# Kernel tuning notes

Measured on AMD Instinct MI355X. Metric: run time of the kernel, lower is better.

The kernel has to match this reference:

```python
import jax, jax.numpy as jnp
import numpy as np

C = 8      # num_channels
H = 512    # dim_hidden
B, S = 32, 1024
EPS = 1e-5


def _layernorm(x, gamma, beta):
    mu = jnp.mean(x, axis=-1, keepdims=True)
    var = jnp.var(x, axis=-1, keepdims=True)
    return (x - mu) * jax.lax.rsqrt(var + EPS) * gamma + beta


def setup_inputs() -> dict:
    key = jax.random.key(0)
    ks = jax.random.split(key, 7)
    x = jax.random.normal(ks[0], (C, B, S, 1), dtype=jnp.float32)
    # per-channel Linear(1,H): torch weight [H,1] -> stacked as [C,H]
    enc_w = jax.random.normal(ks[1], (C, H), dtype=jnp.float32) / jnp.sqrt(1.0)
    enc_b = jax.random.normal(ks[2], (C, H), dtype=jnp.float32) * 0.02
    enc_gamma = jnp.ones((C, H), dtype=jnp.float32)
    enc_beta = jnp.zeros((C, H), dtype=jnp.float32)
    # modulator Linear(C*H -> H): torch weight [H, C*H]
    mod_w = jax.random.normal(ks[3], (H, C * H), dtype=jnp.float32) / jnp.sqrt(C * H)
    mod_b = jax.random.normal(ks[4], (H,), dtype=jnp.float32) * 0.02
    mod_gamma = jnp.ones((H,), dtype=jnp.float32)
    mod_beta = jnp.zeros((H,), dtype=jnp.float32)
    return {
        "x": x,
        "enc_w": enc_w, "enc_b": enc_b,
        "enc_gamma": enc_gamma, "enc_beta": enc_beta,
        "mod_w": mod_w, "mod_b": mod_b,
        "mod_gamma": mod_gamma, "mod_beta": mod_beta,
    }


def reference(x, enc_w, enc_b, enc_gamma, enc_beta, mod_w, mod_b, mod_gamma, mod_beta):
    # per-channel Linear(1,H): h[c,b,s,:] = x[c,b,s,0]*enc_w[c] + enc_b[c]
    h = x * enc_w[:, None, None, :] + enc_b[:, None, None, :]      # [C,B,S,H]
    h = _layernorm(h, enc_gamma[:, None, None, :], enc_beta[:, None, None, :])
    h = jax.nn.gelu(h, approximate=False)
    # concat along last dim in channel order -> [B,S,C*H]
    h = jnp.transpose(h, (1, 2, 0, 3)).reshape(B, S, C * H)
    # channel modulator: Linear + LayerNorm + GELU
    y = jnp.einsum("bsk,hk->bsh", h, mod_w) + mod_b                # [B,S,H]
    y = _layernorm(y, mod_gamma, mod_beta)
    return jax.nn.gelu(y, approximate=False)
```

## Files before the change

kernel.cpp:

```cpp
#include <hip/hip_runtime.h>
#include <hip/hip_bf16.h>
#include <math.h>

#define C_CH 8
#define H_DIM 512
#define BS 32768
#define K_DIM 4096
#define EPS 1e-5f

#define TM 64
#define TK 32
#define NKT (K_DIM / TK)

typedef __bf16 bf16x8 __attribute__((ext_vector_type(8)));
typedef float  floatx4 __attribute__((ext_vector_type(4)));

__device__ __forceinline__ float gelu_fast(float v) {
    float x = v * fmaf(v * v, 0.07135481627f, 1.595769122f);
    float e = __expf(-x);
    return v * __builtin_amdgcn_rcpf(1.0f + e);
}

__global__ __launch_bounds__(256) void conv_w_kernel(const float* __restrict__ w,
                                                     __bf16* __restrict__ o) {
    int gtid  = blockIdx.x * 256 + threadIdx.x;
    int lane  = gtid & 63;
    int chunk = gtid >> 6;
    int kt    = chunk >> 5;
    int ntile = chunk & 31;
    int col   = ntile * 16 + (lane & 15);
    int k     = kt * 32 + (lane >> 4) * 8;
    const float* src = w + (size_t)col * K_DIM + k;
    float4 a = *(const float4*)src;
    float4 b = *(const float4*)(src + 4);
    bf16x8 h;
    h[0] = (__bf16)a.x; h[1] = (__bf16)a.y; h[2] = (__bf16)a.z; h[3] = (__bf16)a.w;
    h[4] = (__bf16)b.x; h[5] = (__bf16)b.y; h[6] = (__bf16)b.z; h[7] = (__bf16)b.w;
    *(bf16x8*)(o + (size_t)gtid * 8) = h;
}

template <int USE_WS>
__global__ __launch_bounds__(256, 2) void fused_gemm_kernel(
    const float* __restrict__ x,
    const float* __restrict__ enc_w,
    const float* __restrict__ enc_b,
    const float* __restrict__ enc_gamma,
    const float* __restrict__ enc_beta,
    const float* __restrict__ mod_w,
    const __bf16* __restrict__ Wb,
    const float* __restrict__ mod_b,
    const float* __restrict__ mod_gamma,
    const float* __restrict__ mod_beta,
    float* __restrict__ out)
{
    __shared__ float stats[C_CH][5];
    __shared__ float pS[C_CH][TM];
    __shared__ float qS[C_CH][TM];
    __shared__ float rS[C_CH][TM];
    __shared__ __align__(16) __bf16 Als[2][TM * TK];
    __shared__ float redS[TM][4];
    __shared__ float redQ[TM][4];
    __shared__ float muS[TM];
    __shared__ float invS[TM];

    const int tid  = threadIdx.x;
    const int wave = tid >> 6;
    const int lane = tid & 63;

    for (int c = wave; c < C_CH; c += 4) {
        float sw = 0.f, sb = 0.f, sww = 0.f, sbb = 0.f, swb = 0.f;
        for (int j = lane; j < H_DIM; j += 64) {
            float w = enc_w[c * H_DIM + j];
            float b = enc_b[c * H_DIM + j];
            sw += w; sb += b;
            sww = fmaf(w, w, sww);
            sbb = fmaf(b, b, sbb);
            swb = fmaf(w, b, swb);
        }
        #pragma unroll
        for (int off = 32; off; off >>= 1) {
            sw  += __shfl_xor(sw,  off);
            sb  += __shfl_xor(sb,  off);
            sww += __shfl_xor(sww, off);
            sbb += __shfl_xor(sbb, off);
            swb += __shfl_xor(swb, off);
        }
        if (lane == 0) {
            const float inv = 1.0f / (float)H_DIM;
            float mw = sw * inv, mb = sb * inv;
            stats[c][0] = mw;
            stats[c][1] = mb;
            stats[c][2] = sww * inv - mw * mw;
            stats[c][3] = sbb * inv - mb * mb;
            stats[c][4] = swb * inv - mw * mb;
        }
    }
    __syncthreads();

    const int row0 = blockIdx.x * TM;
    for (int idx = tid; idx < C_CH * TM; idx += 256) {
        int c = idx >> 6;
        int m = idx & (TM - 1);
        float xv = x[c * BS + row0 + m];
        float mw = stats[c][0], mb = stats[c][1];
        float vw = stats[c][2], vb = stats[c][3], cwb = stats[c][4];
        float var = fmaf(xv, fmaf(xv, vw, 2.0f * cwb), vb);
        float q = rsqrtf(var + EPS);
        float p = xv * q;
        pS[c][m] = p;
        qS[c][m] = q;
        rS[c][m] = -fmaf(p, mw, q * mb);
    }
    __syncthreads();

    const int wn = wave;
    const int lr = lane & 15;
    const int lq = lane >> 4;

    const int arow = tid >> 2;
    const int aq   = tid & 3;
    const int wchunk = arow * 4 + (aq ^ ((arow >> 1) & 3));

    floatx4 acc[4][8];
    #pragma unroll
    for (int i = 0; i < 4; ++i)
        #pragma unroll
        for (int j = 0; j < 8; ++j)
            acc[i][j] = (floatx4){0.f, 0.f, 0.f, 0.f};

    auto stageA = [&](int ktn, __bf16* dst) {
        const int k0 = ktn * TK;
        const int c  = k0 >> 9;
        const int j0 = c * H_DIM + (k0 & (H_DIM - 1)) + aq * 8;
        float p = pS[c][arow], q = qS[c][arow], r = rS[c][arow];
        bf16x8 hv;
        #pragma unroll
        for (int h = 0; h < 2; ++h) {
            float4 w = *(const float4*)(enc_w + j0 + h * 4);
            float4 b = *(const float4*)(enc_b + j0 + h * 4);
            float4 g = *(const float4*)(enc_gamma + j0 + h * 4);
            float4 e = *(const float4*)(enc_beta + j0 + h * 4);
            float fw[4] = {w.x, w.y, w.z, w.w};
            float fb[4] = {b.x, b.y, b.z, b.w};
            float fg[4] = {g.x, g.y, g.z, g.w};
            float fe[4] = {e.x, e.y, e.z, e.w};
            #pragma unroll
            for (int i = 0; i < 4; ++i) {
                float t = fmaf(p, fw[i], fmaf(q, fb[i], r));
                float v = fmaf(t, fg[i], fe[i]);
                hv[h * 4 + i] = (__bf16)gelu_fast(v);
            }
        }
        *(bf16x8*)(dst + wchunk * 8) = hv;
    };

    auto loadB = [&](int ktn, int half, bf16x8* dst) {
        if (USE_WS) {
            const __bf16* base = Wb + ((size_t)(ktn * 32 + wn * 8 + half * 4) * 64 + lane) * 8;
            #pragma unroll
            for (int nt = 0; nt < 4; ++nt)
                dst[nt] = *(const bf16x8*)(base + (size_t)nt * 64 * 8);
        } else {
            const int kk = ktn * 32 + lq * 8;
            #pragma unroll
            for (int nt = 0; nt < 4; ++nt) {
                int col = wn * 128 + (half * 4 + nt) * 16 + lr;
                const float* src = mod_w + (size_t)col * K_DIM + kk;
                float4 a = *(const float4*)src;
                float4 b = *(const float4*)(src + 4);
                bf16x8 h;
                h[0] = (__bf16)a.x; h[1] = (__bf16)a.y; h[2] = (__bf16)a.z; h[3] = (__bf16)a.w;
                h[4] = (__bf16)b.x; h[5] = (__bf16)b.y; h[6] = (__bf16)b.z; h[7] = (__bf16)b.w;
                dst[nt] = h;
            }
        }
    };

    bf16x8 bfrP[4], bfrQ[4];
    loadB(0, 0, bfrP);
    stageA(0, Als[0]);
    __syncthreads();

    for (int kt = 0; kt < NKT; ++kt) {
        loadB(kt, 1, bfrQ);

        if (kt + 1 < NKT) stageA(kt + 1, Als[(kt + 1) & 1]);

        const __bf16* Acur = Als[kt & 1];
        bf16x8 af[4];
        #pragma unroll
        for (int mt = 0; mt < 4; ++mt) {
            int row = mt * 16 + lr;
            int chunk = row * 4 + (lq ^ ((row >> 1) & 3));
            af[mt] = *(const bf16x8*)(Acur + chunk * 8);
        }

        #pragma unroll
        for (int mt = 0; mt < 4; ++mt)
            #pragma unroll
            for (int nt = 0; nt < 4; ++nt)
                acc[mt][nt] = __builtin_amdgcn_mfma_f32_16x16x32_bf16(
                    af[mt], bfrP[nt], acc[mt][nt], 0, 0, 0);

        if (kt + 1 < NKT) loadB(kt + 1, 0, bfrP);

        #pragma unroll
        for (int mt = 0; mt < 4; ++mt)
            #pragma unroll
            for (int nt = 0; nt < 4; ++nt)
                acc[mt][nt + 4] = __builtin_amdgcn_mfma_f32_16x16x32_bf16(
                    af[mt], bfrQ[nt], acc[mt][nt + 4], 0, 0, 0);

        __syncthreads();
    }

    float mbv[8], gv[8], bev[8];
    #pragma unroll
    for (int nt = 0; nt < 8; ++nt) {
        int col = wn * 128 + nt * 16 + lr;
        mbv[nt] = mod_b[col];
        gv[nt]  = mod_gamma[col];
        bev[nt] = mod_beta[col];
    }
    #pragma unroll
    for (int mt = 0; mt < 4; ++mt)
        #pragma unroll
        for (int nt = 0; nt < 8; ++nt)
            #pragma unroll
            for (int r = 0; r < 4; ++r)
                acc[mt][nt][r] += mbv[nt];

    #pragma unroll
    for (int mt = 0; mt < 4; ++mt) {
        #pragma unroll
        for (int r = 0; r < 4; ++r) {
            float s = 0.f, ss = 0.f;
            #pragma unroll
            for (int nt = 0; nt < 8; ++nt) {
                float y = acc[mt][nt][r];
                s += y;
                ss = fmaf(y, y, ss);
            }
            #pragma unroll
            for (int off = 1; off < 16; off <<= 1) {
                s  += __shfl_xor(s,  off);
                ss += __shfl_xor(ss, off);
            }
            if (lr == 0) {
                int row = mt * 16 + lq * 4 + r;
                redS[row][wn] = s;
                redQ[row][wn] = ss;
            }
        }
    }
    __syncthreads();
    if (tid < TM) {
        float s  = redS[tid][0] + redS[tid][1] + redS[tid][2] + redS[tid][3];
        float ss = redQ[tid][0] + redQ[tid][1] + redQ[tid][2] + redQ[tid][3];
        const float inv_n = 1.0f / (float)H_DIM;
        float mu  = s * inv_n;
        float var = ss * inv_n - mu * mu;
        muS[tid]  = mu;
        invS[tid] = rsqrtf(var + EPS);
    }
    __syncthreads();

    #pragma unroll
    for (int mt = 0; mt < 4; ++mt) {
        #pragma unroll
        for (int r = 0; r < 4; ++r) {
            int row = mt * 16 + lq * 4 + r;
            float mu  = muS[row];
            float inv = invS[row];
            float* op = out + (size_t)(row0 + row) * H_DIM;
            #pragma unroll
            for (int nt = 0; nt < 8; ++nt) {
                int col = wn * 128 + nt * 16 + lr;
                float t = fmaf((acc[mt][nt][r] - mu) * inv, gv[nt], bev[nt]);
                op[col] = gelu_fast(t);
            }
        }
    }
}

extern "C" void kernel_launch(void* const* d_in, const int* in_sizes, int n_in,
                              void* d_out, int out_size, void* d_ws, size_t ws_size,
                              hipStream_t stream) {
    const float* x         = (const float*)d_in[0];
    const float* enc_w     = (const float*)d_in[1];
    const float* enc_b     = (const float*)d_in[2];
    const float* enc_gamma = (const float*)d_in[3];
    const float* enc_beta  = (const float*)d_in[4];
    const float* mod_w     = (const float*)d_in[5];
    const float* mod_b     = (const float*)d_in[6];
    const float* mod_gamma = (const float*)d_in[7];
    const float* mod_beta  = (const float*)d_in[8];
    float* out = (float*)d_out;

    const size_t wb_bytes = (size_t)H_DIM * K_DIM * sizeof(__bf16);
    int use_ws = (ws_size >= wb_bytes) ? 1 : 0;
    __bf16* Wb = (__bf16*)d_ws;

    if (use_ws) {
        conv_w_kernel<<<(H_DIM * K_DIM) / (256 * 8), 256, 0, stream>>>(mod_w, Wb);
        fused_gemm_kernel<1><<<BS / TM, 256, 0, stream>>>(
            x, enc_w, enc_b, enc_gamma, enc_beta, mod_w, Wb,
            mod_b, mod_gamma, mod_beta, out);
    } else {
        fused_gemm_kernel<0><<<BS / TM, 256, 0, stream>>>(
            x, enc_w, enc_b, enc_gamma, enc_beta, mod_w, Wb,
            mod_b, mod_gamma, mod_beta, out);
    }
}
```

Measured before the change: 278.0 us.

## Split GEMM block across eight waves, each owning 64 output columns

The block grows from 256 to 512 threads so each of eight waves computes a 64x64 slice of the output instead of four waves computing 64x128. The per-wave accumulator drops from 32 to 16 MFMA tiles. The A-staging, stats and LayerNorm reductions are remapped so each thread does half the work. The goal is fewer registers and more resident waves to hide latency, at the cost of more A-fragment LDS reads per output and more threads per barrier.

```diff
diff --git a/kernel.cpp b/kernel.cpp
--- a/kernel.cpp
+++ b/kernel.cpp
@@ -13,6 +13,7 @@
 #define NKT (K_DIM / TK)
 
 typedef __bf16 bf16x8 __attribute__((ext_vector_type(8)));
+typedef __bf16 bf16x4 __attribute__((ext_vector_type(4)));
 typedef float  floatx4 __attribute__((ext_vector_type(4)));
 
 __device__ __forceinline__ float gelu_fast(float v) {
@@ -40,7 +41,7 @@
 }
 
 template <int USE_WS>
-__global__ __launch_bounds__(256, 2) void fused_gemm_kernel(
+__global__ __launch_bounds__(512, 4) void fused_gemm_kernel(
     const float* __restrict__ x,
     const float* __restrict__ enc_w,
     const float* __restrict__ enc_b,
@@ -58,8 +59,8 @@
     __shared__ float qS[C_CH][TM];
     __shared__ float rS[C_CH][TM];
     __shared__ __align__(16) __bf16 Als[2][TM * TK];
-    __shared__ float redS[TM][4];
-    __shared__ float redQ[TM][4];
+    __shared__ float redS[TM][8];
+    __shared__ float redQ[TM][8];
     __shared__ float muS[TM];
     __shared__ float invS[TM];
 
@@ -67,7 +68,8 @@
     const int wave = tid >> 6;
     const int lane = tid & 63;
 
-    for (int c = wave; c < C_CH; c += 4) {
+    {
+        const int c = wave;
         float sw = 0.f, sb = 0.f, sww = 0.f, sbb = 0.f, swb = 0.f;
         for (int j = lane; j < H_DIM; j += 64) {
             float w = enc_w[c * H_DIM + j];
@@ -98,9 +100,9 @@
     __syncthreads();
 
     const int row0 = blockIdx.x * TM;
-    for (int idx = tid; idx < C_CH * TM; idx += 256) {
-        int c = idx >> 6;
-        int m = idx & (TM - 1);
+    {
+        int c = wave;
+        int m = lane;
         float xv = x[c * BS + row0 + m];
         float mw = stats[c][0], mb = stats[c][1];
         float vw = stats[c][2], vb = stats[c][3], cwb = stats[c][4];
@@ -117,54 +119,51 @@
     const int lr = lane & 15;
     const int lq = lane >> 4;
 
-    const int arow = tid >> 2;
-    const int aq   = tid & 3;
-    const int wchunk = arow * 4 + (aq ^ ((arow >> 1) & 3));
-
-    floatx4 acc[4][8];
+    const int arow  = tid >> 3;
+    const int akq   = (tid >> 1) & 3;
+    const int ahalf = tid & 1;
+    const int wchunk = arow * 4 + (akq ^ ((arow >> 1) & 3));
+
+    floatx4 acc[4][4];
     #pragma unroll
     for (int i = 0; i < 4; ++i)
         #pragma unroll
-        for (int j = 0; j < 8; ++j)
+        for (int j = 0; j < 4; ++j)
             acc[i][j] = (floatx4){0.f, 0.f, 0.f, 0.f};
 
     auto stageA = [&](int ktn, __bf16* dst) {
         const int k0 = ktn * TK;
         const int c  = k0 >> 9;
-        const int j0 = c * H_DIM + (k0 & (H_DIM - 1)) + aq * 8;
+        const int j0 = c * H_DIM + (k0 & (H_DIM - 1)) + akq * 8 + ahalf * 4;
         float p = pS[c][arow], q = qS[c][arow], r = rS[c][arow];
-        bf16x8 hv;
-        #pragma unroll
-        for (int h = 0; h < 2; ++h) {
-            float4 w = *(const float4*)(enc_w + j0 + h * 4);
-            float4 b = *(const float4*)(enc_b + j0 + h * 4);
-            float4 g = *(const float4*)(enc_gamma + j0 + h * 4);
-            float4 e = *(const float4*)(enc_beta + j0 + h * 4);
-            float fw[4] = {w.x, w.y, w.z, w.w};
-            float fb[4] = {b.x, b.y, b.z, b.w};
-            float fg[4] = {g.x, g.y, g.z, g.w};
-            float fe[4] = {e.x, e.y, e.z, e.w};
-            #pragma unroll
-            for (int i = 0; i < 4; ++i) {
-                float t = fmaf(p, fw[i], fmaf(q, fb[i], r));
-                float v = fmaf(t, fg[i], fe[i]);
-                hv[h * 4 + i] = (__bf16)gelu_fast(v);
-            }
-        }
-        *(bf16x8*)(dst + wchunk * 8) = hv;
+        float4 w = *(const float4*)(enc_w + j0);
+        float4 b = *(const float4*)(enc_b + j0);
+        float4 g = *(const float4*)(enc_gamma + j0);
+        float4 e = *(const float4*)(enc_beta + j0);
+        float fw[4] = {w.x, w.y, w.z, w.w};
+        float fb[4] = {b.x, b.y, b.z, b.w};
+        float fg[4] = {g.x, g.y, g.z, g.w};
+        float fe[4] = {e.x, e.y, e.z, e.w};
+        bf16x4 hv;
+        #pragma unroll
+        for (int i = 0; i < 4; ++i) {
+            float t = fmaf(p, fw[i], fmaf(q, fb[i], r));
+            float v = fmaf(t, fg[i], fe[i]);
+            hv[i] = (__bf16)gelu_fast(v);
+        }
+        *(bf16x4*)(dst + wchunk * 8 + ahalf * 4) = hv;
     };
 
     auto loadB = [&](int ktn, int half, bf16x8* dst) {
         if (USE_WS) {
-            const __bf16* base = Wb + ((size_t)(ktn * 32 + wn * 8 + half * 4) * 64 + lane) * 8;
-            #pragma unroll
-            for (int nt = 0; nt < 4; ++nt)
-                dst[nt] = *(const bf16x8*)(base + (size_t)nt * 64 * 8);
+            const __bf16* base = Wb + ((size_t)(ktn * 32 + wn * 4 + half * 2) * 64 + lane) * 8;
+            dst[0] = *(const bf16x8*)(base);
+            dst[1] = *(const bf16x8*)(base + 512);
         } else {
             const int kk = ktn * 32 + lq * 8;
             #pragma unroll
-            for (int nt = 0; nt < 4; ++nt) {
-                int col = wn * 128 + (half * 4 + nt) * 16 + lr;
+            for (int nt = 0; nt < 2; ++nt) {
+                int col = wn * 64 + (half * 2 + nt) * 16 + lr;
                 const float* src = mod_w + (size_t)col * K_DIM + kk;
                 float4 a = *(const float4*)src;
                 float4 b = *(const float4*)(src + 4);
@@ -176,7 +175,7 @@
         }
     };
 
-    bf16x8 bfrP[4], bfrQ[4];
+    bf16x8 bfrP[2], bfrQ[2];
     loadB(0, 0, bfrP);
     stageA(0, Als[0]);
     __syncthreads();
@@ -198,7 +197,7 @@
         #pragma unroll
         for (int mt = 0; mt < 4; ++mt)
             #pragma unroll
-            for (int nt = 0; nt < 4; ++nt)
+            for (int nt = 0; nt < 2; ++nt)
                 acc[mt][nt] = __builtin_amdgcn_mfma_f32_16x16x32_bf16(
                     af[mt], bfrP[nt], acc[mt][nt], 0, 0, 0);
 
@@ -207,17 +206,17 @@
         #pragma unroll
         for (int mt = 0; mt < 4; ++mt)
             #pragma unroll
-            for (int nt = 0; nt < 4; ++nt)
-                acc[mt][nt + 4] = __builtin_amdgcn_mfma_f32_16x16x32_bf16(
-                    af[mt], bfrQ[nt], acc[mt][nt + 4], 0, 0, 0);
+            for (int nt = 0; nt < 2; ++nt)
+                acc[mt][nt + 2] = __builtin_amdgcn_mfma_f32_16x16x32_bf16(
+                    af[mt], bfrQ[nt], acc[mt][nt + 2], 0, 0, 0);
 
         __syncthreads();
     }
 
-    float mbv[8], gv[8], bev[8];
-    #pragma unroll
-    for (int nt = 0; nt < 8; ++nt) {
-        int col = wn * 128 + nt * 16 + lr;
+    float mbv[4], gv[4], bev[4];
+    #pragma unroll
+    for (int nt = 0; nt < 4; ++nt) {
+        int col = wn * 64 + nt * 16 + lr;
         mbv[nt] = mod_b[col];
         gv[nt]  = mod_gamma[col];
         bev[nt] = mod_beta[col];
@@ -225,7 +224,7 @@
     #pragma unroll
     for (int mt = 0; mt < 4; ++mt)
         #pragma unroll
-        for (int nt = 0; nt < 8; ++nt)
+        for (int nt = 0; nt < 4; ++nt)
             #pragma unroll
             for (int r = 0; r < 4; ++r)
                 acc[mt][nt][r] += mbv[nt];
@@ -236,7 +235,7 @@
         for (int r = 0; r < 4; ++r) {
             float s = 0.f, ss = 0.f;
             #pragma unroll
-            for (int nt = 0; nt < 8; ++nt) {
+            for (int nt = 0; nt < 4; ++nt) {
                 float y = acc[mt][nt][r];
                 s += y;
                 ss = fmaf(y, y, ss);
@@ -255,8 +254,12 @@
     }
     __syncthreads();
     if (tid < TM) {
-        float s  = redS[tid][0] + redS[tid][1] + redS[tid][2] + redS[tid][3];
-        float ss = redQ[tid][0] + redQ[tid][1] + redQ[tid][2] + redQ[tid][3];
+        float s = 0.f, ss = 0.f;
+        #pragma unroll
+        for (int w = 0; w < 8; ++w) {
+            s  += redS[tid][w];
+            ss += redQ[tid][w];
+        }
         const float inv_n = 1.0f / (float)H_DIM;
         float mu  = s * inv_n;
         float var = ss * inv_n - mu * mu;
@@ -274,8 +277,8 @@
             float inv = invS[row];
             float* op = out + (size_t)(row0 + row) * H_DIM;
             #pragma unroll
-            for (int nt = 0; nt < 8; ++nt) {
-                int col = wn * 128 + nt * 16 + lr;
+            for (int nt = 0; nt < 4; ++nt) {
+                int col = wn * 64 + nt * 16 + lr;
                 float t = fmaf((acc[mt][nt][r] - mu) * inv, gv[nt], bev[nt]);
                 op[col] = gelu_fast(t);
             }
@@ -303,11 +306,11 @@
 
     if (use_ws) {
         conv_w_kernel<<<(H_DIM * K_DIM) / (256 * 8), 256, 0, stream>>>(mod_w, Wb);
-        fused_gemm_kernel<1><<<BS / TM, 256, 0, stream>>>(
+        fused_gemm_kernel<1><<<BS / TM, 512, 0, stream>>>(
             x, enc_w, enc_b, enc_gamma, enc_beta, mod_w, Wb,
             mod_b, mod_gamma, mod_beta, out);
     } else {
-        fused_gemm_kernel<0><<<BS / TM, 256, 0, stream>>>(
+        fused_gemm_kernel<0><<<BS / TM, 512, 0, stream>>>(
             x, enc_w, enc_b, enc_gamma, enc_beta, mod_w, Wb,
             mod_b, mod_gamma, mod_beta, out);
     }
```

Result: faster. 249.9 us (-10.1%).
